# Kernel tuning notes

Hardware: AMD Instinct MI355X
Metric: run time of the kernel (lower is better)

Reference implementation:

```python
import jax, jax.numpy as jnp
import numpy as np

N_QUBITS = 12
K_STEPS = 6
VOCAB = 32000
D_EMB = 512
N_CLASSES = 8
B = 256
SEQ = 128
DIM = 2 ** N_QUBITS


def apply_1q(psi, U, q):
    # psi: [B, 2^n]; U: [2,2] (shared) or [B,2,2] (per-sample). Apply on wire q
    # (PennyLane convention: wire 0 = most significant axis).
    b = psi.shape[0]
    left, right = 2 ** q, 2 ** (N_QUBITS - q - 1)
    st = psi.reshape(b, left, 2, right)
    if U.ndim == 3:
        st = jnp.einsum('bij,bajr->bair', U, st)
    else:
        st = jnp.einsum('ij,bajr->bair', U, st)
    return st.reshape(b, DIM)


def apply_cnot(psi, c, t):
    b = psi.shape[0]
    st = psi.reshape((b,) + (2,) * N_QUBITS)
    c_ax, t_ax = 1 + c, 1 + t
    c0 = jnp.take(st, 0, axis=c_ax)
    c1 = jnp.take(st, 1, axis=c_ax)
    t_ax2 = t_ax - 1 if t_ax > c_ax else t_ax  # axis shift after take
    c1 = jnp.flip(c1, axis=t_ax2)
    return jnp.stack([c0, c1], axis=c_ax).reshape(b, DIM)


def ry_mat(angle):
    # angle: [B] -> [B,2,2] complex64
    c = jnp.cos(angle / 2)
    s = jnp.sin(angle / 2)
    row0 = jnp.stack([c, -s], axis=-1)
    row1 = jnp.stack([s, c], axis=-1)
    return jnp.stack([row0, row1], axis=-2).astype(jnp.complex64)


def rot_mat(phi, theta, omega):
    # PennyLane Rot(phi, theta, omega) = RZ(omega) RY(theta) RZ(phi)
    c = jnp.cos(theta / 2)
    s = jnp.sin(theta / 2)
    ep = jnp.exp(-0.5j * (phi + omega).astype(jnp.complex64))
    em = jnp.exp(0.5j * (phi - omega).astype(jnp.complex64))
    m = jnp.stack([jnp.stack([ep * c, -em * s]), jnp.stack([jnp.conj(em) * s, jnp.conj(ep) * c])])
    return m.astype(jnp.complex64)


def block(psi, x, theta_k):
    # data reupload RY(x_i), trainable Rot, ring of CNOTs (noiseless)
    for i in range(N_QUBITS):
        psi = apply_1q(psi, ry_mat(x[:, i]), i)
    for i in range(N_QUBITS):
        psi = apply_1q(psi, rot_mat(theta_k[i, 0], theta_k[i, 1], theta_k[i, 2]), i)
    for i in range(N_QUBITS - 1):
        psi = apply_cnot(psi, i, i + 1)
    psi = apply_cnot(psi, N_QUBITS - 1, 0)
    return psi


def z_expvals(psi):
    # <Z_i> for all wires from |psi|^2
    b = psi.shape[0]
    p = (psi.real ** 2 + psi.imag ** 2).reshape((b,) + (2,) * N_QUBITS)
    zs = []
    for i in range(N_QUBITS):
        axes = tuple(ax for ax in range(1, N_QUBITS + 1) if ax != 1 + i)
        m = p.sum(axis=axes)  # [B,2]
        zs.append(m[:, 0] - m[:, 1])
    return jnp.stack(zs, axis=-1)  # [B, n_qubits]


def _forward(input_ids, attention_mask, emb_table, proj_w, proj_b, theta, head_w, head_b):
    # encoder: embed -> masked mean pool -> tanh(linear) * pi
    e = emb_table[input_ids]                              # [B,S,D]
    mask = attention_mask[:, :, None].astype(jnp.float32)
    pooled = (e * mask).sum(axis=1) / jnp.clip(mask.sum(axis=1), 1.0)
    x = jnp.tanh(pooled @ proj_w.T + proj_b) * jnp.float32(np.pi)  # [B, n_qubits]

    b = x.shape[0]
    psi = jnp.zeros((b, DIM), jnp.complex64).at[:, 0].set(1.0)
    readouts = []
    for k in range(K_STEPS):
        psi = block(psi, x, theta[k])
        readouts.append(z_expvals(psi))
    step_readouts = jnp.stack(readouts, axis=0)           # [K,B,n_qubits]
    step_logits = step_readouts @ head_w.T + head_b       # [K,B,n_classes]
    return step_logits, step_readouts, step_logits[-1]


def setup_inputs() -> dict:
    key = jax.random.key(0)
    ks = jax.random.split(key, 6)
    input_ids = jax.random.randint(ks[0], (B, SEQ), 0, VOCAB)
    attention_mask = jnp.ones((B, SEQ), dtype=jnp.int32)
    emb_table = jax.random.normal(ks[1], (VOCAB, D_EMB), jnp.float32)
    emb_table = emb_table.at[0].set(0.0)  # padding_idx=0 row is zeros
    proj_w = jax.random.normal(ks[2], (N_QUBITS, D_EMB), jnp.float32) / np.sqrt(D_EMB)
    proj_b = jnp.zeros((N_QUBITS,), jnp.float32)
    theta = 0.01 * jax.random.normal(ks[3], (K_STEPS, N_QUBITS, 3), jnp.float32)
    head_w = jax.random.normal(ks[4], (N_CLASSES, N_QUBITS), jnp.float32) / np.sqrt(N_QUBITS)
    head_b = jnp.zeros((N_CLASSES,), jnp.float32)
    return {'input_ids': input_ids, 'attention_mask': attention_mask,
            'emb_table': emb_table, 'proj_w': proj_w, 'proj_b': proj_b,
            'theta': theta, 'head_w': head_w, 'head_b': head_b}


def reference(input_ids, attention_mask, emb_table, proj_w, proj_b, theta, head_w, head_b):
    return _forward(input_ids, attention_mask, emb_table, proj_w, proj_b, theta, head_w, head_b)
```

## Files before the change

### kernel.cpp

```cpp
#include <hip/hip_runtime.h>
#include <math.h>

#define NQ 12
#define DIM 4096
#define KS 6
#define BB 256
#define SEQ 128
#define DEMB 512


typedef float f2 __attribute__((ext_vector_type(2)));

#define RG(P, W) { \
    f2 E01 = *(const f2*)&s_u[k][W][0]; \
    f2 E23 = *(const f2*)&s_u[k][W][2]; \
    f2 PR0 = (f2){ E01.x,  E01.x}; \
    f2 PI0 = (f2){-E01.y,  E01.y}; \
    f2 PR1 = (f2){ E23.x,  E23.x}; \
    f2 PI1 = (f2){-E23.y,  E23.y}; \
    _Pragma("unroll") \
    for (int r0 = 0; r0 < 8; ++r0) if (!(r0 & (1 << (P)))) { \
        int r1 = r0 | (1 << (P)); \
        f2 A = a[r0], Bv = a[r1]; \
        f2 As = (f2){A.y, A.x}, Bs = (f2){Bv.y, Bv.x}; \
        a[r0] = PR0*A  + PI0*As + PR1*Bv + PI1*Bs; \
        a[r1] = PR0*Bv - PI0*Bs - PR1*A  + PI1*As; \
    } }

#define BF_PLAIN(v, m) { float p_ = __shfl_xor(v, m, 64); v = v + p_; }
#define BF_SIGN(v, m)  { float p_ = __shfl_xor(v, m, 64); float d_ = v - p_; \
                         v = (lane & m) ? -d_ : d_; }

#define WAVE_FENCE() asm volatile("s_waitcnt lgkmcnt(0)" ::: "memory")

#define BARRIER() { asm volatile("s_waitcnt lgkmcnt(0)" ::: "memory"); \
                    __builtin_amdgcn_s_barrier(); }

__device__ __forceinline__ int swz14(int x) { return x ^ ((x >> 4) & 14); }

__global__ __launch_bounds__(512) void fused_kernel(
    const int* __restrict__ ids, const int* __restrict__ mask,
    const float* __restrict__ emb, const float* __restrict__ pw,
    const float* __restrict__ pb, const float* __restrict__ theta,
    const float* __restrict__ hw, const float* __restrict__ hb,
    float* __restrict__ readouts, float* __restrict__ logits,
    float* __restrict__ last)
{
    __shared__ __align__(16) f2    buf0[DIM];
    __shared__ __align__(16) f2    buf1[DIM];
    __shared__ __align__(16) float s_u[KS][NQ][4];
    __shared__ float  s_red[8][NQ];
    __shared__ float  s_rall[KS][NQ];
    __shared__ float  s_msum[4];
    __shared__ float  s_wred[2][NQ];
    __shared__ float  s_x[NQ];
    __shared__ float  s_hw[8 * NQ];
    __shared__ float  s_hb[8];

    int b = blockIdx.x;
    int tid = threadIdx.x;
    int lane = tid & 63, wave = tid >> 6;

    int*   s_ids = (int*)buf1;
    float* s_m   = (float*)buf1 + SEQ;
    float4* s_part = (float4*)buf0;

    if (tid < SEQ) {
        s_ids[tid] = ids[b * SEQ + tid];
        s_m[tid]   = (float)mask[b * SEQ + tid];
    }
    if (tid >= 256 && tid < 256 + 8 * NQ) s_hw[tid - 256] = hw[tid - 256];
    if (tid >= 384 && tid < 392)          s_hb[tid - 384] = hb[tid - 384];
    __syncthreads();

    {
        int g = tid >> 7, e = tid & 127;
        float4 acc = make_float4(0.f, 0.f, 0.f, 0.f);
        float msum = 0.f;
        #pragma unroll 4
        for (int s = g; s < SEQ; s += 4) {
            float m = s_m[s];
            float4 v = ((const float4*)emb)[(size_t)s_ids[s] * 128 + e];
            acc.x = fmaf(m, v.x, acc.x);
            acc.y = fmaf(m, v.y, acc.y);
            acc.z = fmaf(m, v.z, acc.z);
            acc.w = fmaf(m, v.w, acc.w);
            msum += m;
        }
        __syncthreads();
        s_part[g * 128 + e] = acc;
        if (e == 0) s_msum[g] = msum;
    }
    __syncthreads();

    if (tid < 128) {
        float tm = fmaxf(s_msum[0] + s_msum[1] + s_msum[2] + s_msum[3], 1.f);
        float inv = 1.f / tm;
        float4 p0 = s_part[0 * 128 + tid], p1 = s_part[1 * 128 + tid];
        float4 p2 = s_part[2 * 128 + tid], p3 = s_part[3 * 128 + tid];
        float4 p;
        p.x = (p0.x + p1.x + p2.x + p3.x) * inv;
        p.y = (p0.y + p1.y + p2.y + p3.y) * inv;
        p.z = (p0.z + p1.z + p2.z + p3.z) * inv;
        p.w = (p0.w + p1.w + p2.w + p3.w) * inv;
        float z[NQ];
        #pragma unroll
        for (int i = 0; i < NQ; ++i) {
            float4 w4 = ((const float4*)pw)[i * 128 + tid];
            z[i] = p.x * w4.x + p.y * w4.y + p.z * w4.z + p.w * w4.w;
        }
        #pragma unroll
        for (int i = 0; i < NQ; ++i) {
            #pragma unroll
            for (int off = 32; off > 0; off >>= 1)
                z[i] += __shfl_xor(z[i], off, 64);
        }
        if ((tid & 63) == 0) {
            int w = tid >> 6;
            #pragma unroll
            for (int i = 0; i < NQ; ++i) s_wred[w][i] = z[i];
        }
    }
    __syncthreads();
    if (tid < NQ) {
        float d = pb[tid] + s_wred[0][tid] + s_wred[1][tid];
        s_x[tid] = tanhf(d) * 3.14159274101257324f;
    }
    __syncthreads();

    if (tid < KS * NQ * 4) {
        int k = tid / 48;
        int rem = tid - k * 48;
        int w = rem >> 2, q = rem & 3;
        float ang = s_x[w];
        float cy = cosf(0.5f * ang), sy = sinf(0.5f * ang);
        const float* th = theta + (k * NQ + w) * 3;
        float phi = th[0], te = th[1], om = th[2];
        float ct = cosf(0.5f * te), st = sinf(0.5f * te);
        float a1 = -0.5f * (phi + om);
        float a2 =  0.5f * (phi - om);
        float ar =  cosf(a1) * ct, ai =  sinf(a1) * ct;
        float br = -cosf(a2) * st, bi = -sinf(a2) * st;
        float x1 = (q & 1) ? ai : ar;
        float x2 = (q & 1) ? bi : br;
        float E  = (q & 2) ? (x2 * cy - x1 * sy) : (x1 * cy + x2 * sy);
        s_u[k][w][q] = E;
    }

    int T8 = tid << 3;
    int baseA  = swz14(T8);
    int baseA4 = baseA >> 1;
    int addrB[8], addrC[8], addrD[8], idxP[8];
    #pragma unroll
    for (int r = 0; r < 8; ++r) {
        addrB[r] = swz14((lane & 7) + 8 * r + 64 * (lane >> 3) + 512 * wave);
        addrC[r] = swz14(lane + 64 * r + 512 * wave);
        int jD   = lane + 64 * wave + 512 * r;
        addrD[r] = swz14(jD);
        int b0 = (jD >> 11) & 1;
        int pref = b0, outv = 0;
        for (int w = 1; w < NQ; ++w) {
            pref ^= (jD >> (11 - w)) & 1;
            outv |= pref << (11 - w);
        }
        outv |= (b0 ^ pref) << 11;
        idxP[r] = swz14(outv);
    }
    int w0b = wave & 1, w1b = (wave >> 1) & 1, w2b = (wave >> 2) & 1;
    int wall = w0b ^ w1b ^ w2b;

    f2 a[8];
    #pragma unroll
    for (int r = 0; r < 8; ++r) a[r] = (f2){0.f, 0.f};
    if (tid == 0) a[0].x = 1.f;
    __syncthreads();

    for (int k = 0; k < KS; ++k) {
        RG(0, 11) RG(1, 10) RG(2, 9)

        #pragma unroll
        for (int i = 0; i < 4; ++i)
            ((float4*)buf0)[baseA4 ^ i] =
                make_float4(a[2*i].x, a[2*i].y, a[2*i+1].x, a[2*i+1].y);
        WAVE_FENCE();
        #pragma unroll
        for (int r = 0; r < 8; ++r) a[r] = buf0[addrB[r]];

        RG(0, 8) RG(1, 7) RG(2, 6)

        #pragma unroll
        for (int r = 0; r < 8; ++r) buf0[addrB[r]] = a[r];
        WAVE_FENCE();
        #pragma unroll
        for (int r = 0; r < 8; ++r) a[r] = buf0[addrC[r]];

        RG(0, 5) RG(1, 4) RG(2, 3)

        #pragma unroll
        for (int r = 0; r < 8; ++r) buf0[addrC[r]] = a[r];
        BARRIER();
        #pragma unroll
        for (int r = 0; r < 8; ++r) a[r] = buf0[addrD[r]];

        RG(0, 2) RG(1, 1) RG(2, 0)

        #pragma unroll
        for (int r = 0; r < 8; ++r) buf1[idxP[r]] = a[r];

        {
            float p[8];
            #pragma unroll
            for (int r = 0; r < 8; ++r)
                p[r] = a[r].x * a[r].x + a[r].y * a[r].y;
            float Q1 = (p[0]+p[1]+p[6]+p[7]) - (p[2]+p[3]+p[4]+p[5]);
            float Q2 = (p[0]+p[3]+p[5]+p[6]) - (p[1]+p[2]+p[4]+p[7]);
            float Q0 = (p[0]+p[3]+p[4]+p[7]) - (p[1]+p[2]+p[5]+p[6]);
            float q1 = Q1, q2p = Q2, q0 = Q0;
            BF_PLAIN(q1,32) BF_PLAIN(q1,16) BF_PLAIN(q1,8)
            BF_PLAIN(q1,4)  BF_PLAIN(q1,2)  BF_PLAIN(q1,1)
            BF_PLAIN(q2p,32) BF_PLAIN(q2p,16) BF_PLAIN(q2p,8)
            BF_PLAIN(q2p,4)  BF_PLAIN(q2p,2)  BF_PLAIN(q2p,1)
            BF_SIGN(q0,32) BF_SIGN(q0,16) BF_SIGN(q0,8)
            BF_SIGN(q0,4)  BF_SIGN(q0,2)  BF_SIGN(q0,1)
            float c = Q2;
            BF_SIGN(c,32);
            float w6v = c; BF_PLAIN(w6v,16) BF_PLAIN(w6v,8) BF_PLAIN(w6v,4)
                           BF_PLAIN(w6v,2)  BF_PLAIN(w6v,1)
            BF_SIGN(c,16);
            float w7v = c; BF_PLAIN(w7v,8) BF_PLAIN(w7v,4)
                           BF_PLAIN(w7v,2) BF_PLAIN(w7v,1)
            BF_SIGN(c,8);
            float w8v = c; BF_PLAIN(w8v,4) BF_PLAIN(w8v,2) BF_PLAIN(w8v,1)
            BF_SIGN(c,4);
            float w9v = c; BF_PLAIN(w9v,2) BF_PLAIN(w9v,1)
            BF_SIGN(c,2);
            float w10v = c; BF_PLAIN(w10v,1)
            BF_SIGN(c,1);
            if (lane == 0) {
                float* sr = s_red[wave];
                sr[0]  = wall ? -q0  : q0;
                sr[1]  = q1;
                sr[2]  = q2p;
                sr[3]  = w2b ? -q2p : q2p;
                sr[4]  = (w1b ^ w2b) ? -q2p : q2p;
                sr[5]  = wall ? -q2p : q2p;
                sr[6]  = wall ? -w6v : w6v;
                sr[7]  = wall ? -w7v : w7v;
                sr[8]  = wall ? -w8v : w8v;
                sr[9]  = wall ? -w9v : w9v;
                sr[10] = wall ? -w10v : w10v;
                sr[11] = wall ? -c   : c;
            }
        }

        BARRIER();
        #pragma unroll
        for (int i = 0; i < 4; ++i) {
            float4 v = ((float4*)buf1)[baseA4 ^ i];
            a[2*i]   = (f2){v.x, v.y};
            a[2*i+1] = (f2){v.z, v.w};
        }

        if (tid < NQ) {
            float s = 0.f;
            #pragma unroll
            for (int w2 = 0; w2 < 8; ++w2) s += s_red[w2][tid];
            s_rall[k][tid] = s;
        }
    }

    BARRIER();
    if (tid < KS * NQ) {
        int k = tid / NQ, i = tid - k * NQ;
        readouts[(k * BB + b) * NQ + i] = s_rall[k][i];
    }
    if (tid >= 128 && tid < 128 + KS * 8) {
        int t = tid - 128;
        int k = t >> 3, c = t & 7;
        float acc2 = s_hb[c];
        #pragma unroll
        for (int i = 0; i < NQ; ++i)
            acc2 = fmaf(s_rall[k][i], s_hw[c * NQ + i], acc2);
        logits[(k * BB + b) * 8 + c] = acc2;
        if (k == KS - 1) last[b * 8 + c] = acc2;
    }
}

extern "C" void kernel_launch(void* const* d_in, const int* in_sizes, int n_in,
                              void* d_out, int out_size, void* d_ws, size_t ws_size,
                              hipStream_t stream) {
    const int*   ids   = (const int*)d_in[0];
    const int*   mask  = (const int*)d_in[1];
    const float* emb   = (const float*)d_in[2];
    const float* pw    = (const float*)d_in[3];
    const float* pb    = (const float*)d_in[4];
    const float* theta = (const float*)d_in[5];
    const float* hw    = (const float*)d_in[6];
    const float* hb    = (const float*)d_in[7];
    float* out = (float*)d_out;

    float* readouts = out + KS * BB * 8;
    float* last     = out + KS * BB * 8 + KS * BB * NQ;

    fused_kernel<<<BB, 512, 0, stream>>>(ids, mask, emb, pw, pb, theta,
                                         hw, hb, readouts, out, last);
}
```

Measured before the change: 129.7 us.

## Defer per-step Z-expectation reductions until after all circuit steps

Each thread now writes its three partial parity sums for every step into a new shared array instead of running cross-lane butterfly reductions inside the step loop. After the loop, six waves each reduce one step's partials in parallel, first across waves with signs and then across lanes with butterflies. This takes the reduction shuffles and the small serial sum off the critical path of the step loop. In exchange it uses about 36 KB more LDS, which may lower occupancy.

Measured after the change: 126.1 us. 1.03x faster.

```diff
diff --git a/kernel.cpp b/kernel.cpp
--- a/kernel.cpp
+++ b/kernel.cpp
@@ -48,8 +48,8 @@
 {
     __shared__ __align__(16) f2    buf0[DIM];
     __shared__ __align__(16) f2    buf1[DIM];
+    __shared__ __align__(16) float s_pq[KS][3][512];
     __shared__ __align__(16) float s_u[KS][NQ][4];
-    __shared__ float  s_red[8][NQ];
     __shared__ float  s_rall[KS][NQ];
     __shared__ float  s_msum[4];
     __shared__ float  s_wred[2][NQ];
@@ -166,8 +166,6 @@
         outv |= (b0 ^ pref) << 11;
         idxP[r] = swz14(outv);
     }
-    int w0b = wave & 1, w1b = (wave >> 1) & 1, w2b = (wave >> 2) & 1;
-    int wall = w0b ^ w1b ^ w2b;
 
     f2 a[8];
     #pragma unroll
@@ -215,42 +213,9 @@
             float Q1 = (p[0]+p[1]+p[6]+p[7]) - (p[2]+p[3]+p[4]+p[5]);
             float Q2 = (p[0]+p[3]+p[5]+p[6]) - (p[1]+p[2]+p[4]+p[7]);
             float Q0 = (p[0]+p[3]+p[4]+p[7]) - (p[1]+p[2]+p[5]+p[6]);
-            float q1 = Q1, q2p = Q2, q0 = Q0;
-            BF_PLAIN(q1,32) BF_PLAIN(q1,16) BF_PLAIN(q1,8)
-            BF_PLAIN(q1,4)  BF_PLAIN(q1,2)  BF_PLAIN(q1,1)
-            BF_PLAIN(q2p,32) BF_PLAIN(q2p,16) BF_PLAIN(q2p,8)
-            BF_PLAIN(q2p,4)  BF_PLAIN(q2p,2)  BF_PLAIN(q2p,1)
-            BF_SIGN(q0,32) BF_SIGN(q0,16) BF_SIGN(q0,8)
-            BF_SIGN(q0,4)  BF_SIGN(q0,2)  BF_SIGN(q0,1)
-            float c = Q2;
-            BF_SIGN(c,32);
-            float w6v = c; BF_PLAIN(w6v,16) BF_PLAIN(w6v,8) BF_PLAIN(w6v,4)
-                           BF_PLAIN(w6v,2)  BF_PLAIN(w6v,1)
-            BF_SIGN(c,16);
-            float w7v = c; BF_PLAIN(w7v,8) BF_PLAIN(w7v,4)
-                           BF_PLAIN(w7v,2) BF_PLAIN(w7v,1)
-            BF_SIGN(c,8);
-            float w8v = c; BF_PLAIN(w8v,4) BF_PLAIN(w8v,2) BF_PLAIN(w8v,1)
-            BF_SIGN(c,4);
-            float w9v = c; BF_PLAIN(w9v,2) BF_PLAIN(w9v,1)
-            BF_SIGN(c,2);
-            float w10v = c; BF_PLAIN(w10v,1)
-            BF_SIGN(c,1);
-            if (lane == 0) {
-                float* sr = s_red[wave];
-                sr[0]  = wall ? -q0  : q0;
-                sr[1]  = q1;
-                sr[2]  = q2p;
-                sr[3]  = w2b ? -q2p : q2p;
-                sr[4]  = (w1b ^ w2b) ? -q2p : q2p;
-                sr[5]  = wall ? -q2p : q2p;
-                sr[6]  = wall ? -w6v : w6v;
-                sr[7]  = wall ? -w7v : w7v;
-                sr[8]  = wall ? -w8v : w8v;
-                sr[9]  = wall ? -w9v : w9v;
-                sr[10] = wall ? -w10v : w10v;
-                sr[11] = wall ? -c   : c;
-            }
+            s_pq[k][0][tid] = Q0;
+            s_pq[k][1][tid] = Q1;
+            s_pq[k][2][tid] = Q2;
         }
 
         BARRIER();
@@ -260,12 +225,67 @@
             a[2*i]   = (f2){v.x, v.y};
             a[2*i+1] = (f2){v.z, v.w};
         }
-
-        if (tid < NQ) {
-            float s = 0.f;
-            #pragma unroll
-            for (int w2 = 0; w2 < 8; ++w2) s += s_red[w2][tid];
-            s_rall[k][tid] = s;
+    }
+
+    BARRIER();
+    if (wave < KS) {
+        int k = wave;
+        float sA = 0.f, sB0 = 0.f, sB1 = 0.f, sB2 = 0.f, sB3 = 0.f, sC = 0.f;
+        #pragma unroll
+        for (int w2 = 0; w2 < 8; ++w2) {
+            float Q0v = s_pq[k][0][(w2 << 6) | lane];
+            float Q1v = s_pq[k][1][(w2 << 6) | lane];
+            float Q2v = s_pq[k][2][(w2 << 6) | lane];
+            int w2b_  = (w2 >> 2) & 1;
+            int w12_  = ((w2 >> 1) ^ (w2 >> 2)) & 1;
+            int wall_ = (w2 ^ (w2 >> 1) ^ (w2 >> 2)) & 1;
+            sA  += Q1v;
+            sB0 += Q2v;
+            sB1 += w2b_  ? -Q2v : Q2v;
+            sB2 += w12_  ? -Q2v : Q2v;
+            sB3 += wall_ ? -Q2v : Q2v;
+            sC  += wall_ ? -Q0v : Q0v;
+        }
+        float v5s = sB3;
+        BF_PLAIN(sA,32)  BF_PLAIN(sA,16)  BF_PLAIN(sA,8)
+        BF_PLAIN(sA,4)   BF_PLAIN(sA,2)   BF_PLAIN(sA,1)
+        BF_PLAIN(sB0,32) BF_PLAIN(sB0,16) BF_PLAIN(sB0,8)
+        BF_PLAIN(sB0,4)  BF_PLAIN(sB0,2)  BF_PLAIN(sB0,1)
+        BF_PLAIN(sB1,32) BF_PLAIN(sB1,16) BF_PLAIN(sB1,8)
+        BF_PLAIN(sB1,4)  BF_PLAIN(sB1,2)  BF_PLAIN(sB1,1)
+        BF_PLAIN(sB2,32) BF_PLAIN(sB2,16) BF_PLAIN(sB2,8)
+        BF_PLAIN(sB2,4)  BF_PLAIN(sB2,2)  BF_PLAIN(sB2,1)
+        BF_PLAIN(v5s,32) BF_PLAIN(v5s,16) BF_PLAIN(v5s,8)
+        BF_PLAIN(v5s,4)  BF_PLAIN(v5s,2)  BF_PLAIN(v5s,1)
+        BF_SIGN(sC,32) BF_SIGN(sC,16) BF_SIGN(sC,8)
+        BF_SIGN(sC,4)  BF_SIGN(sC,2)  BF_SIGN(sC,1)
+        float c = sB3;
+        BF_SIGN(c,32);
+        float w6v = c; BF_PLAIN(w6v,16) BF_PLAIN(w6v,8) BF_PLAIN(w6v,4)
+                       BF_PLAIN(w6v,2)  BF_PLAIN(w6v,1)
+        BF_SIGN(c,16);
+        float w7v = c; BF_PLAIN(w7v,8) BF_PLAIN(w7v,4)
+                       BF_PLAIN(w7v,2) BF_PLAIN(w7v,1)
+        BF_SIGN(c,8);
+        float w8v = c; BF_PLAIN(w8v,4) BF_PLAIN(w8v,2) BF_PLAIN(w8v,1)
+        BF_SIGN(c,4);
+        float w9v = c; BF_PLAIN(w9v,2) BF_PLAIN(w9v,1)
+        BF_SIGN(c,2);
+        float w10v = c; BF_PLAIN(w10v,1)
+        BF_SIGN(c,1);
+        if (lane == 0) {
+            s_rall[k][0]  = sC;
+            s_rall[k][1]  = sA;
+            s_rall[k][2]  = sB0;
+            s_rall[k][3]  = sB1;
+            s_rall[k][4]  = sB2;
+            s_rall[k][5]  = v5s;
+            s_rall[k][6]  = w6v;
+            s_rall[k][7]  = w7v;
+            s_rall[k][8]  = w8v;
+            s_rall[k][9]  = w9v;
+            s_rall[k][10] = w10v;
+            s_rall[k][11] = c;
         }
     }
 
```
